# Kernel tuning notes

Hardware: AMD Instinct MI355X
Metric: run time of the kernel (lower is better)

## Reference

```python
import jax, jax.numpy as jnp
import numpy as np

N = 50000
E = 1_600_000
S = 0.05  # param init scale


def setup_inputs() -> dict:
    key = jax.random.key(0)
    ks = jax.random.split(key, 12)
    return {
        "x": jax.random.normal(ks[0], (N, 1), jnp.float32),
        "edge_index": jax.random.randint(ks[1], (2, E), 0, N, dtype=jnp.int32),
        "W_gcn": jax.random.normal(ks[2], (2, 128), jnp.float32) * S,
        "b_gcn": jax.random.normal(ks[3], (128,), jnp.float32) * S,
        "W_sage_l": jax.random.normal(ks[4], (128, 128), jnp.float32) * S,
        "b_sage_l": jax.random.normal(ks[5], (128,), jnp.float32) * S,
        "W_sage_r": jax.random.normal(ks[6], (128, 128), jnp.float32) * S,
        "W_v1": jax.random.normal(ks[7], (128, 64), jnp.float32) * S,
        "b_v1": jax.random.normal(ks[8], (64,), jnp.float32) * S,
        "W_v2": jax.random.normal(ks[9], (64, 1), jnp.float32) * S,
        "b_v2": jax.random.normal(ks[10], (1,), jnp.float32) * S,
    }


def reference(x, edge_index, W_gcn, b_gcn, W_sage_l, b_sage_l, W_sage_r,
              W_v1, b_v1, W_v2, b_v2):
    n = x.shape[0]
    src, dst = edge_index[0], edge_index[1]
    ones_e = jnp.ones(src.shape, x.dtype)

    # degree feature: out-degree of source nodes (torch_geometric.utils.degree)
    deg0 = jax.ops.segment_sum(ones_e, src, num_segments=n)
    xin = jnp.concatenate([x, deg0[:, None]], axis=-1)  # [N, 2]

    # --- GCNConv(2,128): add self-loops, symmetric normalization ---
    loop = jnp.arange(n, dtype=src.dtype)
    s2 = jnp.concatenate([src, loop])
    d2 = jnp.concatenate([dst, loop])
    deg = jax.ops.segment_sum(jnp.ones(d2.shape, x.dtype), d2, num_segments=n)
    dinv = jnp.where(deg > 0, jax.lax.rsqrt(deg), 0.0)
    h = xin @ W_gcn                      # [N, 128]
    norm = dinv[s2] * dinv[d2]           # [E+N]
    z1 = jax.ops.segment_sum(norm[:, None] * h[s2], d2, num_segments=n) + b_gcn
    a1 = jax.nn.relu(z1)

    # --- SAGEConv(128,128): mean neighbor aggregation + root weight ---
    cnt = jax.ops.segment_sum(ones_e, dst, num_segments=n)
    agg = jax.ops.segment_sum(a1[src], dst, num_segments=n)
    agg = agg / jnp.maximum(cnt, 1.0)[:, None]
    a2 = agg @ W_sage_l + b_sage_l + a1 @ W_sage_r

    # --- value head ---
    v = jax.nn.relu(a2 @ W_v1 + b_v1) @ W_v2 + b_v2  # [N, 1]
    return jnp.sum(v)
```

## Files before the change

kernel.cpp:

```cpp
#include <hip/hip_runtime.h>

#define NCH 128
#define TILE 2048
#define SUBCAP 3072
#define SCHUNK 2048
#define SNODES 32
#define HSTRIDE 264

typedef __attribute__((ext_vector_type(8))) short bf16x8;
typedef __attribute__((ext_vector_type(4))) float f32x4;

__device__ inline unsigned short f2bf(float f) {
  unsigned int u = __builtin_bit_cast(unsigned int, f);
  unsigned int r = u + 0x7fffu + ((u >> 16) & 1u);
  return (unsigned short)(r >> 16);
}

__device__ inline int xcc_id() {
  int x;
  asm volatile("s_getreg_b32 %0, hwreg(HW_REG_XCC_ID)" : "=s"(x));
  return x & 7;
}

__global__ void prep_w_kernel(const float* __restrict__ Wl, const float* __restrict__ Wr,
                              const float* __restrict__ Wv1,
                              unsigned short* fw1, unsigned short* fw2,
                              int* __restrict__ gcur1, int* __restrict__ gcur2,
                              float* out, const float* __restrict__ bv2, int n) {
  int i = blockIdx.x * blockDim.x + threadIdx.x;
  if (i < 32768) {
    int j = i & 7, l = (i >> 3) & 63, s = (i >> 9) & 7, t = i >> 12;
    int k = s * 32 + (l >> 4) * 8 + j;
    int nn = t * 16 + (l & 15);
    float v = (k < 128) ? Wl[k * 128 + nn] : Wr[(k - 128) * 128 + nn];
    fw1[i] = f2bf(v);
  }
  if (i < 8192) {
    int j = i & 7, l = (i >> 3) & 63, s = (i >> 9) & 3, t = i >> 11;
    int k = s * 32 + (l >> 4) * 8 + j;
    int nn = t * 16 + (l & 15);
    fw2[i] = f2bf(Wv1[k * 64 + nn]);
  }
  if (i < 2048) gcur1[i] = i * SUBCAP;
  else if (i < 4096) gcur2[i - 2048] = (i - 2048) * SUBCAP;
  if (i == 4096) out[0] = (float)n * bv2[0];
}

__global__ __launch_bounds__(256) void partition_kernel(
    const int* __restrict__ src, const int* __restrict__ dst,
    int* __restrict__ gcur1, int* __restrict__ gcur2,
    unsigned int* __restrict__ part, unsigned short* __restrict__ part_s, int ne) {
  __shared__ int h1[256], h2[256], c1[256], c2[256];
  int t = threadIdx.x, b = blockIdx.x;
  h1[t] = 0; h2[t] = 0;
  __syncthreads();
  int base = b * TILE;
  int lim = min(base + TILE, ne);
  for (int i = base + t; i < lim; i += 256) {
    atomicAdd(&h1[((unsigned)dst[i]) >> 8], 1);
    atomicAdd(&h2[((unsigned)src[i]) >> 8], 1);
  }
  __syncthreads();
  int xcd = xcc_id();
  c1[t] = atomicAdd(&gcur1[xcd * 256 + t], h1[t]);
  c2[t] = atomicAdd(&gcur2[xcd * 256 + t], h2[t]);
  __syncthreads();
  for (int i = base + t; i < lim; i += 256) {
    unsigned d = (unsigned)dst[i], s = (unsigned)src[i];
    int p1 = atomicAdd(&c1[d >> 8], 1);
    part[p1] = (d << 16) | s;
    int p2 = atomicAdd(&c2[s >> 8], 1);
    part_s[p2] = (unsigned short)s;
  }
}

__global__ __launch_bounds__(256) void bucket_kernel(
    const unsigned int* __restrict__ part, const unsigned short* __restrict__ part_s,
    const int* __restrict__ gcur1, const int* __restrict__ gcur2,
    int* __restrict__ row_beg, int* __restrict__ deg, int* __restrict__ csr_src,
    const float* __restrict__ x, float* __restrict__ p2, int n) {
  __shared__ int h[256], h2[256], sc[256], c[256];
  __shared__ int outBase;
  int t = threadIdx.x;
  int b = blockIdx.x;
  h[t] = 0; h2[t] = 0;
  if (t == 0) outBase = 0;
  __syncthreads();
#pragma unroll
  for (int xz = 0; xz < 8; xz++) {
    int rb = (xz * 256 + b) * SUBCAP, re = gcur1[xz * 256 + b];
    for (int i = rb + t; i < re; i += 256)
      atomicAdd(&h[(part[i] >> 16) & 255], 1);
    int sb = (xz * 256 + b) * SUBCAP, se = gcur2[xz * 256 + b];
    for (int i = sb + t; i < se; i += 256)
      atomicAdd(&h2[part_s[i] & 255], 1);
  }
  __syncthreads();
  int hv = h[t];
  sc[t] = hv;
  __syncthreads();
  for (int off = 1; off < 256; off <<= 1) {
    int u = (t >= off) ? sc[t - off] : 0;
    __syncthreads();
    sc[t] += u;
    __syncthreads();
  }
  int bucketBase = b * 8192;
  int excl = sc[t] - hv;
  int node = b * 256 + t;
  if (node < n) { row_beg[node] = bucketBase + excl; deg[node] = hv; }
  c[t] = bucketBase + excl;
  __syncthreads();
#pragma unroll
  for (int xz = 0; xz < 8; xz++) {
    int rb = (xz * 256 + b) * SUBCAP, re = gcur1[xz * 256 + b];
    for (int i = rb + t; i < re; i += 256) {
      unsigned key = part[i];
      int pos = atomicAdd(&c[(key >> 16) & 255], 1);
      csr_src[pos] = (int)(key & 0xFFFFu);
    }
  }
  if (node < n) {
    float dinv = rsqrtf((float)hv + 1.0f);
    p2[2 * node]     = dinv * x[node];
    p2[2 * node + 1] = dinv * (float)h2[t];
  }
}

__global__ __launch_bounds__(256) void gcn_t_kernel(
    const int* __restrict__ row_beg, const int* __restrict__ deg,
    const int* __restrict__ csr_src,
    const float* __restrict__ p2, float2* __restrict__ tvec, int npad, int n) {
  int wid = (blockIdx.x * blockDim.x + threadIdx.x) >> 6;
  int lane = threadIdx.x & 63;
  if (wid >= npad) return;
  if (wid >= n) { if (lane == 0) tvec[wid] = make_float2(0.f, 0.f); return; }
  int beg = row_beg[wid], dg = deg[wid], end = beg + dg;
  float s0 = 0.0f, s1 = 0.0f;
  for (int k = beg + lane; k < end; k += 64) {
    int s = csr_src[k];
    float2 v = *reinterpret_cast<const float2*>(p2 + 2 * (size_t)s);
    s0 += v.x; s1 += v.y;
  }
#pragma unroll
  for (int off = 1; off < 64; off <<= 1) {
    s0 += __shfl_xor(s0, off, 64);
    s1 += __shfl_xor(s1, off, 64);
  }
  float dinv = rsqrtf((float)dg + 1.0f);
  float2 self = *reinterpret_cast<const float2*>(p2 + 2 * (size_t)wid);
  if (lane == 0)
    tvec[wid] = make_float2(dinv * (s0 + self.x), dinv * (s1 + self.y));
}

__global__ __launch_bounds__(256) void sage_kernel(
    const int* __restrict__ row_beg, const int* __restrict__ deg,
    const int* __restrict__ csr_src, const float2* __restrict__ tvec,
    const float* __restrict__ Wg, const float* __restrict__ bg,
    unsigned int* __restrict__ agg32, int n) {
  __shared__ float2 sE[SCHUNK];
  __shared__ int sR[SNODES + 1];
  int tid = threadIdx.x, lane = tid & 63, w = tid >> 6;
  int node0 = blockIdx.x * SNODES;
  if (tid <= SNODES) {
    int node = node0 + tid;
    int v;
    if (tid == SNODES) {
      int last = min(node, n) - 1;
      v = (last >= 0) ? row_beg[last] + deg[last] : 0;
    } else if (node < n) {
      v = row_beg[node];
    } else {
      v = (n > 0) ? row_beg[n - 1] + deg[n - 1] : 0;
    }
    sR[tid] = v;
  }
  __syncthreads();
  int base = sR[0], endAll = sR[SNODES];

  int c0 = 2 * lane, c1 = c0 + 1;
  float w00 = Wg[c0], w10 = Wg[NCH + c0], b0 = bg[c0];
  float w01 = Wg[c1], w11 = Wg[NCH + c1], b1 = bg[c1];
  float ax[8], ay[8];
#pragma unroll
  for (int i = 0; i < 8; i++) { ax[i] = 0.f; ay[i] = 0.f; }

  for (int cbeg = base; cbeg < endAll; cbeg += SCHUNK) {
    int cend = min(cbeg + SCHUNK, endAll);
    __syncthreads();
    for (int k = cbeg + tid; k < cend; k += 256)
      sE[k - cbeg] = tvec[csr_src[k]];
    __syncthreads();
#pragma unroll
    for (int i = 0; i < 8; i++) {
      int nd = w * 8 + i;
      int rb = max(sR[nd], cbeg) - cbeg;
      int re = min(sR[nd + 1], cend) - cbeg;
      int k = rb;
      for (; k + 3 < re; k += 4) {
        float2 tA = sE[k], tB = sE[k + 1], tC = sE[k + 2], tD = sE[k + 3];
        ax[i] += fmaxf(fmaf(tA.x, w00, fmaf(tA.y, w10, b0)), 0.f)
               + fmaxf(fmaf(tB.x, w00, fmaf(tB.y, w10, b0)), 0.f)
               + fmaxf(fmaf(tC.x, w00, fmaf(tC.y, w10, b0)), 0.f)
               + fmaxf(fmaf(tD.x, w00, fmaf(tD.y, w10, b0)), 0.f);
        ay[i] += fmaxf(fmaf(tA.x, w01, fmaf(tA.y, w11, b1)), 0.f)
               + fmaxf(fmaf(tB.x, w01, fmaf(tB.y, w11, b1)), 0.f)
               + fmaxf(fmaf(tC.x, w01, fmaf(tC.y, w11, b1)), 0.f)
               + fmaxf(fmaf(tD.x, w01, fmaf(tD.y, w11, b1)), 0.f);
      }
      for (; k < re; k++) {
        float2 tA = sE[k];
        ax[i] += fmaxf(fmaf(tA.x, w00, fmaf(tA.y, w10, b0)), 0.f);
        ay[i] += fmaxf(fmaf(tA.x, w01, fmaf(tA.y, w11, b1)), 0.f);
      }
    }
  }
#pragma unroll
  for (int i = 0; i < 8; i++) {
    int nd = w * 8 + i;
    int cnt = sR[nd + 1] - sR[nd];
    float inv = 1.0f / (float)(cnt > 1 ? cnt : 1);
    agg32[(size_t)(node0 + nd) * 64 + lane] =
        (unsigned int)f2bf(ax[i] * inv) | ((unsigned int)f2bf(ay[i] * inv) << 16);
  }
}

__global__ __launch_bounds__(256) void head_kernel(
    const unsigned short* __restrict__ agg, const float2* __restrict__ tvec,
    const float* __restrict__ Wg, const float* __restrict__ bg,
    const unsigned short* __restrict__ fw1, const unsigned short* __restrict__ fw2,
    const float* __restrict__ bl, const float* __restrict__ bv1,
    const float* __restrict__ Wv2, float* __restrict__ out, int n) {
  __shared__ __align__(16) unsigned short sA[64 * HSTRIDE];
  __shared__ float sT[128];
  __shared__ float sRed[4];
  int tid = threadIdx.x;
  int lane = tid & 63;
  int w = tid >> 6;
  int m16 = lane & 15;
  int quad = lane >> 4;
  int node0 = blockIdx.x * 64;

  const uint4* g = reinterpret_cast<const uint4*>(agg + (size_t)node0 * NCH);
  for (int c = tid; c < 1024; c += 256) {
    int row = c >> 4, off = c & 15;
    *reinterpret_cast<uint4*>(&sA[row * HSTRIDE + off * 8]) = g[row * 16 + off];
  }
  if (tid < 128) sT[tid] = reinterpret_cast<const float*>(tvec + node0)[tid];
  __syncthreads();

  {
    int cp = tid & 63, r0 = tid >> 6;
    int c0 = 2 * cp, c1 = c0 + 1;
    float w00 = Wg[c0], w10 = Wg[NCH + c0], b0 = bg[c0];
    float w01 = Wg[c1], w11 = Wg[NCH + c1], b1 = bg[c1];
#pragma unroll
    for (int i = 0; i < 16; i++) {
      int row = r0 + 4 * i;
      float t0 = sT[2 * row], t1 = sT[2 * row + 1];
      float z0 = fmaxf(fmaf(t0, w00, fmaf(t1, w10, b0)), 0.f);
      float z1 = fmaxf(fmaf(t0, w01, fmaf(t1, w11, b1)), 0.f);
      *reinterpret_cast<unsigned int*>(&sA[row * HSTRIDE + 128 + 2 * cp]) =
          (unsigned int)f2bf(z0) | ((unsigned int)f2bf(z1) << 16);
    }
  }

  bf16x8 b1f[2][8];
  const bf16x8* f1 = reinterpret_cast<const bf16x8*>(fw1);
#pragma unroll
  for (int p = 0; p < 2; p++)
#pragma unroll
    for (int s = 0; s < 8; s++)
      b1f[p][s] = f1[((w * 2 + p) * 8 + s) * 64 + lane];

  f32x4 acc[4][2];
#pragma unroll
  for (int mt = 0; mt < 4; mt++)
#pragma unroll
    for (int p = 0; p < 2; p++) acc[mt][p] = (f32x4)0.0f;

  __syncthreads();

#pragma unroll
  for (int s = 0; s < 8; s++) {
#pragma unroll
    for (int mt = 0; mt < 4; mt++) {
      bf16x8 aF = *reinterpret_cast<const bf16x8*>(
          &sA[(mt * 16 + m16) * HSTRIDE + s * 32 + quad * 8]);
#pragma unroll
      for (int p = 0; p < 2; p++)
        acc[mt][p] = __builtin_amdgcn_mfma_f32_16x16x32_bf16(aF, b1f[p][s],
                                                             acc[mt][p], 0, 0, 0);
    }
  }

  float blv[2];
#pragma unroll
  for (int p = 0; p < 2; p++) blv[p] = bl[(w * 2 + p) * 16 + m16];
  __syncthreads();
#pragma unroll
  for (int mt = 0; mt < 4; mt++)
#pragma unroll
    for (int p = 0; p < 2; p++) {
      int col = (w * 2 + p) * 16 + m16;
#pragma unroll
      for (int r = 0; r < 4; r++) {
        int row = mt * 16 + quad * 4 + r;
        sA[row * HSTRIDE + col] = f2bf(acc[mt][p][r] + blv[p]);
      }
    }
  __syncthreads();

  bf16x8 b2f[4];
  const bf16x8* f2 = reinterpret_cast<const bf16x8*>(fw2);
#pragma unroll
  for (int s = 0; s < 4; s++) b2f[s] = f2[(w * 4 + s) * 64 + lane];

  f32x4 acc2[4];
#pragma unroll
  for (int mt = 0; mt < 4; mt++) acc2[mt] = (f32x4)0.0f;

#pragma unroll
  for (int s = 0; s < 4; s++) {
#pragma unroll
    for (int mt = 0; mt < 4; mt++) {
      bf16x8 aF = *reinterpret_cast<const bf16x8*>(
          &sA[(mt * 16 + m16) * HSTRIDE + s * 32 + quad * 8]);
      acc2[mt] = __builtin_amdgcn_mfma_f32_16x16x32_bf16(aF, b2f[s], acc2[mt], 0, 0, 0);
    }
  }

  int c2 = w * 16 + m16;
  float bvj = bv1[c2], w2 = Wv2[c2];
  float vsum = 0.0f;
#pragma unroll
  for (int mt = 0; mt < 4; mt++)
#pragma unroll
    for (int r = 0; r < 4; r++) {
      int node = node0 + mt * 16 + quad * 4 + r;
      if (node < n) vsum += fmaxf(acc2[mt][r] + bvj, 0.0f) * w2;
    }
#pragma unroll
  for (int off = 1; off < 64; off <<= 1) vsum += __shfl_xor(vsum, off, 64);
  if (lane == 0) sRed[w] = vsum;
  __syncthreads();
  if (tid == 0) atomicAdd(out, sRed[0] + sRed[1] + sRed[2] + sRed[3]);
}

extern "C" void kernel_launch(void* const* d_in, const int* in_sizes, int n_in,
                              void* d_out, int out_size, void* d_ws, size_t ws_size,
                              hipStream_t stream) {
  const float* x   = (const float*)d_in[0];
  const int*   ei  = (const int*)d_in[1];
  const float* Wg  = (const float*)d_in[2];
  const float* bg  = (const float*)d_in[3];
  const float* Wl  = (const float*)d_in[4];
  const float* bl  = (const float*)d_in[5];
  const float* Wr  = (const float*)d_in[6];
  const float* Wv1 = (const float*)d_in[7];
  const float* bv1 = (const float*)d_in[8];
  const float* Wv2 = (const float*)d_in[9];
  const float* bv2 = (const float*)d_in[10];
  float* out = (float*)d_out;

  int n  = in_sizes[0];
  int E_ = in_sizes[1] / 2;
  int npad = ((n + 63) / 64) * 64;
  int B1 = (E_ + TILE - 1) / TILE;
  const int* src = ei;
  const int* dst = ei + E_;

  char* base = (char*)d_ws;
  unsigned short* agg = (unsigned short*)base;  base += (size_t)npad * NCH * 2;
  float2* tvec    = (float2*)base;              base += (size_t)npad * 8;
  unsigned short* fw1 = (unsigned short*)base;  base += 32768 * 2;
  unsigned short* fw2 = (unsigned short*)base;  base += 8192 * 2;
  float* p2       = (float*)base;               base += (size_t)n * 2 * 4;
  int* gcur1      = (int*)base;                 base += 2048 * 4;
  int* gcur2      = (int*)base;                 base += 2048 * 4;
  unsigned int* part = (unsigned int*)base;     base += (size_t)2048 * SUBCAP * 4;
  int* row_beg    = (int*)base;                 base += (size_t)n * 4;
  int* deg        = (int*)base;                 base += (size_t)n * 4;
  int* csr_src    = (int*)base;                 base += (size_t)256 * 8192 * 4;
  unsigned short* part_s = (unsigned short*)base;

  prep_w_kernel<<<128, 256, 0, stream>>>(Wl, Wr, Wv1, fw1, fw2, gcur1, gcur2,
                                         out, bv2, n);
  partition_kernel<<<B1, 256, 0, stream>>>(src, dst, gcur1, gcur2, part, part_s, E_);
  bucket_kernel<<<256, 256, 0, stream>>>(part, part_s, gcur1, gcur2,
                                         row_beg, deg, csr_src, x, p2, n);

  int wave_blocks = npad / 4;
  gcn_t_kernel<<<wave_blocks, 256, 0, stream>>>(row_beg, deg, csr_src, p2,
                                                tvec, npad, n);
  sage_kernel<<<npad / SNODES, 256, 0, stream>>>(row_beg, deg, csr_src, tvec,
                                                 Wg, bg, (unsigned int*)agg, n);
  head_kernel<<<npad / 64, 256, 0, stream>>>(agg, tvec, Wg, bg, fw1, fw2,
                                             bl, bv1, Wv2, out, n);
}
```

Before: 205.7 us.

## Fuse SAGE mean aggregation into head kernel via shared-memory tile

Merges the SAGE neighbor-aggregation kernel and the dense head kernel into one kernel that handles 64 nodes per block. The aggregated bf16 features are written straight into the shared-memory A tile instead of a global buffer, which removes one launch and the global write and read of the N x 128 aggregate. In exchange each block uses more shared memory (gather chunk plus head tile) and holds 16 accumulators per thread. Block count is halved, so there are fewer waves to hide gather latency.

```diff
diff --git a/kernel.cpp b/kernel.cpp
--- a/kernel.cpp
+++ b/kernel.cpp
@@ -4,7 +4,6 @@
 #define TILE 2048
 #define SUBCAP 3072
 #define SCHUNK 2048
-#define SNODES 32
 #define HSTRIDE 264
 
 typedef __attribute__((ext_vector_type(8))) short bf16x8;
@@ -80,11 +79,9 @@
     int* __restrict__ row_beg, int* __restrict__ deg, int* __restrict__ csr_src,
     const float* __restrict__ x, float* __restrict__ p2, int n) {
   __shared__ int h[256], h2[256], sc[256], c[256];
-  __shared__ int outBase;
   int t = threadIdx.x;
   int b = blockIdx.x;
   h[t] = 0; h2[t] = 0;
-  if (t == 0) outBase = 0;
   __syncthreads();
 #pragma unroll
   for (int xz = 0; xz < 8; xz++) {
@@ -153,19 +150,26 @@
     tvec[wid] = make_float2(dinv * (s0 + self.x), dinv * (s1 + self.y));
 }
 
-__global__ __launch_bounds__(256) void sage_kernel(
+__global__ __launch_bounds__(256) void sage_head_kernel(
     const int* __restrict__ row_beg, const int* __restrict__ deg,
     const int* __restrict__ csr_src, const float2* __restrict__ tvec,
     const float* __restrict__ Wg, const float* __restrict__ bg,
-    unsigned int* __restrict__ agg32, int n) {
+    const unsigned short* __restrict__ fw1, const unsigned short* __restrict__ fw2,
+    const float* __restrict__ bl, const float* __restrict__ bv1,
+    const float* __restrict__ Wv2, float* __restrict__ out, int n) {
   __shared__ float2 sE[SCHUNK];
-  __shared__ int sR[SNODES + 1];
+  __shared__ int sR[65];
+  __shared__ __align__(16) unsigned short sA[64 * HSTRIDE];
+  __shared__ float sT[128];
+  __shared__ float sRed[4];
   int tid = threadIdx.x, lane = tid & 63, w = tid >> 6;
-  int node0 = blockIdx.x * SNODES;
-  if (tid <= SNODES) {
+  int m16 = lane & 15, quad = lane >> 4;
+  int node0 = blockIdx.x * 64;
+
+  if (tid <= 64) {
     int node = node0 + tid;
     int v;
-    if (tid == SNODES) {
+    if (tid == 64) {
       int last = min(node, n) - 1;
       v = (last >= 0) ? row_beg[last] + deg[last] : 0;
     } else if (node < n) {
@@ -175,15 +179,16 @@
     }
     sR[tid] = v;
   }
-  __syncthreads();
-  int base = sR[0], endAll = sR[SNODES];
-
-  int c0 = 2 * lane, c1 = c0 + 1;
-  float w00 = Wg[c0], w10 = Wg[NCH + c0], b0 = bg[c0];
-  float w01 = Wg[c1], w11 = Wg[NCH + c1], b1 = bg[c1];
-  float ax[8], ay[8];
-#pragma unroll
-  for (int i = 0; i < 8; i++) { ax[i] = 0.f; ay[i] = 0.f; }
+  if (tid >= 128) sT[tid - 128] = reinterpret_cast<const float*>(tvec + node0)[tid - 128];
+  __syncthreads();
+  int base = sR[0], endAll = sR[64];
+
+  int ch0 = 2 * lane, ch1 = ch0 + 1;
+  float w00 = Wg[ch0], w10 = Wg[NCH + ch0], bb0 = bg[ch0];
+  float w01 = Wg[ch1], w11 = Wg[NCH + ch1], bb1 = bg[ch1];
+  float ax[16], ay[16];
+#pragma unroll
+  for (int i = 0; i < 16; i++) { ax[i] = 0.f; ay[i] = 0.f; }
 
   for (int cbeg = base; cbeg < endAll; cbeg += SCHUNK) {
     int cend = min(cbeg + SCHUNK, endAll);
@@ -192,74 +197,47 @@
       sE[k - cbeg] = tvec[csr_src[k]];
     __syncthreads();
 #pragma unroll
-    for (int i = 0; i < 8; i++) {
-      int nd = w * 8 + i;
+    for (int i = 0; i < 16; i++) {
+      int nd = w * 16 + i;
       int rb = max(sR[nd], cbeg) - cbeg;
       int re = min(sR[nd + 1], cend) - cbeg;
       int k = rb;
       for (; k + 3 < re; k += 4) {
         float2 tA = sE[k], tB = sE[k + 1], tC = sE[k + 2], tD = sE[k + 3];
-        ax[i] += fmaxf(fmaf(tA.x, w00, fmaf(tA.y, w10, b0)), 0.f)
-               + fmaxf(fmaf(tB.x, w00, fmaf(tB.y, w10, b0)), 0.f)
-               + fmaxf(fmaf(tC.x, w00, fmaf(tC.y, w10, b0)), 0.f)
-               + fmaxf(fmaf(tD.x, w00, fmaf(tD.y, w10, b0)), 0.f);
-        ay[i] += fmaxf(fmaf(tA.x, w01, fmaf(tA.y, w11, b1)), 0.f)
-               + fmaxf(fmaf(tB.x, w01, fmaf(tB.y, w11, b1)), 0.f)
-               + fmaxf(fmaf(tC.x, w01, fmaf(tC.y, w11, b1)), 0.f)
-               + fmaxf(fmaf(tD.x, w01, fmaf(tD.y, w11, b1)), 0.f);
+        ax[i] += fmaxf(fmaf(tA.x, w00, fmaf(tA.y, w10, bb0)), 0.f)
+               + fmaxf(fmaf(tB.x, w00, fmaf(tB.y, w10, bb0)), 0.f)
+               + fmaxf(fmaf(tC.x, w00, fmaf(tC.y, w10, bb0)), 0.f)
+               + fmaxf(fmaf(tD.x, w00, fmaf(tD.y, w10, bb0)), 0.f);
+        ay[i] += fmaxf(fmaf(tA.x, w01, fmaf(tA.y, w11, bb1)), 0.f)
+               + fmaxf(fmaf(tB.x, w01, fmaf(tB.y, w11, bb1)), 0.f)
+               + fmaxf(fmaf(tC.x, w01, fmaf(tC.y, w11, bb1)), 0.f)
+               + fmaxf(fmaf(tD.x, w01, fmaf(tD.y, w11, bb1)), 0.f);
       }
       for (; k < re; k++) {
         float2 tA = sE[k];
-        ax[i] += fmaxf(fmaf(tA.x, w00, fmaf(tA.y, w10, b0)), 0.f);
-        ay[i] += fmaxf(fmaf(tA.x, w01, fmaf(tA.y, w11, b1)), 0.f);
+        ax[i] += fmaxf(fmaf(tA.x, w00, fmaf(tA.y, w10, bb0)), 0.f);
+        ay[i] += fmaxf(fmaf(tA.x, w01, fmaf(tA.y, w11, bb1)), 0.f);
       }
     }
   }
-#pragma unroll
-  for (int i = 0; i < 8; i++) {
-    int nd = w * 8 + i;
+
+#pragma unroll
+  for (int i = 0; i < 16; i++) {
+    int nd = w * 16 + i;
     int cnt = sR[nd + 1] - sR[nd];
     float inv = 1.0f / (float)(cnt > 1 ? cnt : 1);
-    agg32[(size_t)(node0 + nd) * 64 + lane] =
+    *reinterpret_cast<unsigned int*>(&sA[nd * HSTRIDE + ch0]) =
         (unsigned int)f2bf(ax[i] * inv) | ((unsigned int)f2bf(ay[i] * inv) << 16);
   }
-}
-
-__global__ __launch_bounds__(256) void head_kernel(
-    const unsigned short* __restrict__ agg, const float2* __restrict__ tvec,
-    const float* __restrict__ Wg, const float* __restrict__ bg,
-    const unsigned short* __restrict__ fw1, const unsigned short* __restrict__ fw2,
-    const float* __restrict__ bl, const float* __restrict__ bv1,
-    const float* __restrict__ Wv2, float* __restrict__ out, int n) {
-  __shared__ __align__(16) unsigned short sA[64 * HSTRIDE];
-  __shared__ float sT[128];
-  __shared__ float sRed[4];
-  int tid = threadIdx.x;
-  int lane = tid & 63;
-  int w = tid >> 6;
-  int m16 = lane & 15;
-  int quad = lane >> 4;
-  int node0 = blockIdx.x * 64;
-
-  const uint4* g = reinterpret_cast<const uint4*>(agg + (size_t)node0 * NCH);
-  for (int c = tid; c < 1024; c += 256) {
-    int row = c >> 4, off = c & 15;
-    *reinterpret_cast<uint4*>(&sA[row * HSTRIDE + off * 8]) = g[row * 16 + off];
-  }
-  if (tid < 128) sT[tid] = reinterpret_cast<const float*>(tvec + node0)[tid];
-  __syncthreads();
 
   {
-    int cp = tid & 63, r0 = tid >> 6;
-    int c0 = 2 * cp, c1 = c0 + 1;
-    float w00 = Wg[c0], w10 = Wg[NCH + c0], b0 = bg[c0];
-    float w01 = Wg[c1], w11 = Wg[NCH + c1], b1 = bg[c1];
+    int cp = lane, r0 = w;
 #pragma unroll
     for (int i = 0; i < 16; i++) {
       int row = r0 + 4 * i;
       float t0 = sT[2 * row], t1 = sT[2 * row + 1];
-      float z0 = fmaxf(fmaf(t0, w00, fmaf(t1, w10, b0)), 0.f);
-      float z1 = fmaxf(fmaf(t0, w01, fmaf(t1, w11, b1)), 0.f);
+      float z0 = fmaxf(fmaf(t0, w00, fmaf(t1, w10, bb0)), 0.f);
+      float z1 = fmaxf(fmaf(t0, w01, fmaf(t1, w11, bb1)), 0.f);
       *reinterpret_cast<unsigned int*>(&sA[row * HSTRIDE + 128 + 2 * cp]) =
           (unsigned int)f2bf(z0) | ((unsigned int)f2bf(z1) << 16);
     }
@@ -371,7 +349,6 @@
   const int* dst = ei + E_;
 
   char* base = (char*)d_ws;
-  unsigned short* agg = (unsigned short*)base;  base += (size_t)npad * NCH * 2;
   float2* tvec    = (float2*)base;              base += (size_t)npad * 8;
   unsigned short* fw1 = (unsigned short*)base;  base += 32768 * 2;
   unsigned short* fw2 = (unsigned short*)base;  base += 8192 * 2;
@@ -393,8 +370,7 @@
   int wave_blocks = npad / 4;
   gcn_t_kernel<<<wave_blocks, 256, 0, stream>>>(row_beg, deg, csr_src, p2,
                                                 tvec, npad, n);
-  sage_kernel<<<npad / SNODES, 256, 0, stream>>>(row_beg, deg, csr_src, tvec,
-                                                 Wg, bg, (unsigned int*)agg, n);
-  head_kernel<<<npad / 64, 256, 0, stream>>>(agg, tvec, Wg, bg, fw1, fw2,
-                                             bl, bv1, Wv2, out, n);
-}
+  sage_head_kernel<<<npad / 64, 256, 0, stream>>>(row_beg, deg, csr_src, tvec,
+                                                  Wg, bg, fw1, fw2,
+                                                  bl, bv1, Wv2, out, n);
+}
```

After: 215.1 us. 1.05x slower.

## Split bucket kernel into dst and src halves; use 16-lane groups per node in GCN

Applied to the files above, without the earlier changes.

The bucket kernel now runs 512 blocks. The first 256 build the dst CSR, and the second 256 compute source out-degree histograms in parallel instead of serially in the same block. A small new p2_kernel computes the normalized node features from the degrees. gcn_t_kernel now gives each node a 16-lane subgroup instead of a whole 64-lane wave, which suits average degrees around 32 and cuts wasted lanes and shuffle work. This adds one extra kernel launch and an outdeg buffer round-trip through memory.

```diff
diff --git a/kernel.cpp b/kernel.cpp
--- a/kernel.cpp
+++ b/kernel.cpp
@@ -78,52 +78,65 @@
     const unsigned int* __restrict__ part, const unsigned short* __restrict__ part_s,
     const int* __restrict__ gcur1, const int* __restrict__ gcur2,
     int* __restrict__ row_beg, int* __restrict__ deg, int* __restrict__ csr_src,
-    const float* __restrict__ x, float* __restrict__ p2, int n) {
-  __shared__ int h[256], h2[256], sc[256], c[256];
-  __shared__ int outBase;
+    int* __restrict__ outdeg, int n) {
+  __shared__ int h[256], sc[256], c[256];
   int t = threadIdx.x;
   int b = blockIdx.x;
-  h[t] = 0; h2[t] = 0;
-  if (t == 0) outBase = 0;
-  __syncthreads();
-#pragma unroll
-  for (int xz = 0; xz < 8; xz++) {
-    int rb = (xz * 256 + b) * SUBCAP, re = gcur1[xz * 256 + b];
-    for (int i = rb + t; i < re; i += 256)
-      atomicAdd(&h[(part[i] >> 16) & 255], 1);
-    int sb = (xz * 256 + b) * SUBCAP, se = gcur2[xz * 256 + b];
-    for (int i = sb + t; i < se; i += 256)
-      atomicAdd(&h2[part_s[i] & 255], 1);
-  }
-  __syncthreads();
-  int hv = h[t];
-  sc[t] = hv;
-  __syncthreads();
-  for (int off = 1; off < 256; off <<= 1) {
-    int u = (t >= off) ? sc[t - off] : 0;
-    __syncthreads();
-    sc[t] += u;
-    __syncthreads();
-  }
-  int bucketBase = b * 8192;
-  int excl = sc[t] - hv;
-  int node = b * 256 + t;
-  if (node < n) { row_beg[node] = bucketBase + excl; deg[node] = hv; }
-  c[t] = bucketBase + excl;
-  __syncthreads();
-#pragma unroll
-  for (int xz = 0; xz < 8; xz++) {
-    int rb = (xz * 256 + b) * SUBCAP, re = gcur1[xz * 256 + b];
-    for (int i = rb + t; i < re; i += 256) {
-      unsigned key = part[i];
-      int pos = atomicAdd(&c[(key >> 16) & 255], 1);
-      csr_src[pos] = (int)(key & 0xFFFFu);
-    }
-  }
-  if (node < n) {
-    float dinv = rsqrtf((float)hv + 1.0f);
-    p2[2 * node]     = dinv * x[node];
-    p2[2 * node + 1] = dinv * (float)h2[t];
+  h[t] = 0;
+  __syncthreads();
+  if (b < 256) {
+#pragma unroll
+    for (int xz = 0; xz < 8; xz++) {
+      int rb = (xz * 256 + b) * SUBCAP, re = gcur1[xz * 256 + b];
+      for (int i = rb + t; i < re; i += 256)
+        atomicAdd(&h[(part[i] >> 16) & 255], 1);
+    }
+    __syncthreads();
+    int hv = h[t];
+    sc[t] = hv;
+    __syncthreads();
+    for (int off = 1; off < 256; off <<= 1) {
+      int u = (t >= off) ? sc[t - off] : 0;
+      __syncthreads();
+      sc[t] += u;
+      __syncthreads();
+    }
+    int bucketBase = b * 8192;
+    int excl = sc[t] - hv;
+    int node = b * 256 + t;
+    if (node < n) { row_beg[node] = bucketBase + excl; deg[node] = hv; }
+    c[t] = bucketBase + excl;
+    __syncthreads();
+#pragma unroll
+    for (int xz = 0; xz < 8; xz++) {
+      int rb = (xz * 256 + b) * SUBCAP, re = gcur1[xz * 256 + b];
+      for (int i = rb + t; i < re; i += 256) {
+        unsigned key = part[i];
+        int pos = atomicAdd(&c[(key >> 16) & 255], 1);
+        csr_src[pos] = (int)(key & 0xFFFFu);
+      }
+    }
+  } else {
+    int bs = b - 256;
+#pragma unroll
+    for (int xz = 0; xz < 8; xz++) {
+      int sb = (xz * 256 + bs) * SUBCAP, se = gcur2[xz * 256 + bs];
+      for (int i = sb + t; i < se; i += 256)
+        atomicAdd(&h[part_s[i] & 255], 1);
+    }
+    __syncthreads();
+    int node = bs * 256 + t;
+    if (node < n) outdeg[node] = h[t];
+  }
+}
+
+__global__ void p2_kernel(const float* __restrict__ x, const int* __restrict__ outdeg,
+                          const int* __restrict__ deg, float* __restrict__ p2, int n) {
+  int i = blockIdx.x * blockDim.x + threadIdx.x;
+  if (i < n) {
+    float dinv = rsqrtf((float)deg[i] + 1.0f);
+    p2[2 * i]     = dinv * x[i];
+    p2[2 * i + 1] = dinv * (float)outdeg[i];
   }
 }
 
@@ -131,26 +144,33 @@
     const int* __restrict__ row_beg, const int* __restrict__ deg,
     const int* __restrict__ csr_src,
     const float* __restrict__ p2, float2* __restrict__ tvec, int npad, int n) {
-  int wid = (blockIdx.x * blockDim.x + threadIdx.x) >> 6;
-  int lane = threadIdx.x & 63;
+  int tid = threadIdx.x;
+  int lane = tid & 63;
+  int sl = lane & 15, g = lane >> 4;
+  int wid = blockIdx.x * 16 + (tid >> 6) * 4 + g;
   if (wid >= npad) return;
-  if (wid >= n) { if (lane == 0) tvec[wid] = make_float2(0.f, 0.f); return; }
-  int beg = row_beg[wid], dg = deg[wid], end = beg + dg;
+  int beg = 0, dg = 0;
+  if (wid < n) { beg = row_beg[wid]; dg = deg[wid]; }
   float s0 = 0.0f, s1 = 0.0f;
-  for (int k = beg + lane; k < end; k += 64) {
+  for (int k = beg + sl; k < beg + dg; k += 16) {
     int s = csr_src[k];
     float2 v = *reinterpret_cast<const float2*>(p2 + 2 * (size_t)s);
     s0 += v.x; s1 += v.y;
   }
 #pragma unroll
-  for (int off = 1; off < 64; off <<= 1) {
+  for (int off = 1; off < 16; off <<= 1) {
     s0 += __shfl_xor(s0, off, 64);
     s1 += __shfl_xor(s1, off, 64);
   }
-  float dinv = rsqrtf((float)dg + 1.0f);
-  float2 self = *reinterpret_cast<const float2*>(p2 + 2 * (size_t)wid);
-  if (lane == 0)
-    tvec[wid] = make_float2(dinv * (s0 + self.x), dinv * (s1 + self.y));
+  if (sl == 0) {
+    if (wid < n) {
+      float dinv = rsqrtf((float)dg + 1.0f);
+      float2 self = *reinterpret_cast<const float2*>(p2 + 2 * (size_t)wid);
+      tvec[wid] = make_float2(dinv * (s0 + self.x), dinv * (s1 + self.y));
+    } else {
+      tvec[wid] = make_float2(0.f, 0.f);
+    }
+  }
 }
 
 __global__ __launch_bounds__(256) void sage_kernel(
@@ -381,18 +401,19 @@
   unsigned int* part = (unsigned int*)base;     base += (size_t)2048 * SUBCAP * 4;
   int* row_beg    = (int*)base;                 base += (size_t)n * 4;
   int* deg        = (int*)base;                 base += (size_t)n * 4;
+  int* outdeg     = (int*)base;                 base += (size_t)n * 4;
   int* csr_src    = (int*)base;                 base += (size_t)256 * 8192 * 4;
   unsigned short* part_s = (unsigned short*)base;
 
   prep_w_kernel<<<128, 256, 0, stream>>>(Wl, Wr, Wv1, fw1, fw2, gcur1, gcur2,
                                          out, bv2, n);
   partition_kernel<<<B1, 256, 0, stream>>>(src, dst, gcur1, gcur2, part, part_s, E_);
-  bucket_kernel<<<256, 256, 0, stream>>>(part, part_s, gcur1, gcur2,
-                                         row_beg, deg, csr_src, x, p2, n);
-
-  int wave_blocks = npad / 4;
-  gcn_t_kernel<<<wave_blocks, 256, 0, stream>>>(row_beg, deg, csr_src, p2,
-                                                tvec, npad, n);
+  bucket_kernel<<<512, 256, 0, stream>>>(part, part_s, gcur1, gcur2,
+                                         row_beg, deg, csr_src, outdeg, n);
+  p2_kernel<<<(n + 255) / 256, 256, 0, stream>>>(x, outdeg, deg, p2, n);
+
+  gcn_t_kernel<<<npad / 16, 256, 0, stream>>>(row_beg, deg, csr_src, p2,
+                                              tvec, npad, n);
   sage_kernel<<<npad / SNODES, 256, 0, stream>>>(row_beg, deg, csr_src, tvec,
                                                  Wg, bg, (unsigned int*)agg, n);
   head_kernel<<<npad / 64, 256, 0, stream>>>(agg, tvec, Wg, bg, fw1, fw2,
```

Result: faster. 194.8 us, median of 2 (-5.3%).
